# Optimization experiments

Hardware: AMD Instinct MI355X
Metric: run time of the kernel (lower is better)

## Reference

```python
import jax, jax.numpy as jnp
import numpy as np

B, T, S, E, H, F = 4, 1024, 1024, 512, 8, 2048
D = E // H  # head_dim = 64
SCALE = D ** -0.5
EPS = 1e-5


def setup_inputs() -> dict:
    key = jax.random.key(0)
    ks = jax.random.split(key, 16)
    w = lambda k, shape: jax.random.normal(k, shape, jnp.float32) * 0.02
    inp = {
        'tgt': jax.random.normal(ks[0], (B, T, E), jnp.float32),
        'memory': jax.random.normal(ks[1], (B, S, E), jnp.float32),
    }
    for i, n in enumerate(['sWq', 'sWk', 'sWv', 'sWo', 'cWq', 'cWk', 'cWv', 'cWo']):
        inp[n] = w(ks[2 + i], (E, E))
    for n in ['sbq', 'sbk', 'sbv', 'sbo', 'cbq', 'cbk', 'cbv', 'cbo']:
        inp[n] = jnp.zeros((E,), jnp.float32)
    inp['fW1'] = w(ks[10], (E, F)); inp['fb1'] = jnp.zeros((F,), jnp.float32)
    inp['fW2'] = w(ks[11], (F, E)); inp['fb2'] = jnp.zeros((E,), jnp.float32)
    for n in ['g1', 'g2', 'g3']:
        inp[n] = jnp.ones((E,), jnp.float32)
    for n in ['be1', 'be2', 'be3']:
        inp[n] = jnp.zeros((E,), jnp.float32)
    return inp


def _ln(x, g, b):
    mu = jnp.mean(x, axis=-1, keepdims=True)
    var = jnp.mean(jnp.square(x - mu), axis=-1, keepdims=True)
    return (x - mu) * jax.lax.rsqrt(var + EPS) * g + b


def _mha(xq, xkv, Wq, bq, Wk, bk, Wv, bv, Wo, bo):
    # dense-equivalent of full N^2 edge-list attention (softmax over source nodes per target)
    Bq, Tq, _ = xq.shape
    Skv = xkv.shape[1]
    q = (xq @ Wq + bq).reshape(Bq, Tq, H, D)
    k = (xkv @ Wk + bk).reshape(Bq, Skv, H, D)
    v = (xkv @ Wv + bv).reshape(Bq, Skv, H, D)
    scores = jnp.einsum('bthd,bshd->bhts', q, k) * SCALE
    wts = jax.nn.softmax(scores, axis=-1)
    out = jnp.einsum('bhts,bshd->bthd', wts, v).reshape(Bq, Tq, E)
    return out @ Wo + bo


def reference(tgt, memory,
              sWq, sbq, sWk, sbk, sWv, sbv, sWo, sbo,
              cWq, cbq, cWk, cbk, cWv, cbv, cWo, cbo,
              fW1, fb1, fW2, fb2,
              g1, be1, g2, be2, g3, be3):
    # post-norm decoder layer: self-attn -> cross-attn -> FFN (dropout=0 eval)
    x = _ln(tgt + _mha(tgt, tgt, sWq, sbq, sWk, sbk, sWv, sbv, sWo, sbo), g1, be1)
    x = _ln(x + _mha(x, memory, cWq, cbq, cWk, cbk, cWv, cbv, cWo, cbo), g2, be2)
    ff = jax.nn.relu(x @ fW1 + fb1) @ fW2 + fb2
    x = _ln(x + ff, g3, be3)
    return x
```

## Files before the change

### kernel.cpp

```cpp
#include <hip/hip_runtime.h>

typedef unsigned short ushort_t;
typedef short short8 __attribute__((ext_vector_type(8)));
typedef float float4v __attribute__((ext_vector_type(4)));

__device__ __forceinline__ float bf2f(ushort_t u) {
    union { unsigned int i; float f; } x; x.i = ((unsigned int)u) << 16; return x.f;
}
__device__ __forceinline__ ushort_t f2bf(float f) {
    unsigned int u = __float_as_uint(f);
    unsigned int r = (u + 0x7FFFu + ((u >> 16) & 1u)) >> 16;
    return (ushort_t)r;
}
__device__ __forceinline__ void store_out(float* p, float v) { *p = v; }
__device__ __forceinline__ void store_out(ushort_t* p, float v) { *p = f2bf(v); }

__device__ __forceinline__ void gll16(const ushort_t* g, ushort_t* l) {
    __builtin_amdgcn_global_load_lds(
        (const __attribute__((address_space(1))) void*)g,
        (__attribute__((address_space(3))) void*)l, 16, 0, 0);
}

__global__ void detect_dtype(const ushort_t* __restrict__ tgt, int* __restrict__ flag) {
    __shared__ int red[256];
    const int tid = threadIdx.x;
    int p = 0;
    for (int i = tid; i < 512; i += 256) {
        ushort_t u = tgt[i];
        int e = (u >> 7) & 0xFF;
        if (u == 0 || (e >= 100 && e <= 140)) ++p;
    }
    red[tid] = p; __syncthreads();
    for (int off = 128; off > 0; off >>= 1) {
        if (tid < off) red[tid] += red[tid + off];
        __syncthreads();
    }
    if (tid == 0) flag[0] = (red[0] >= 480) ? 1 : 0;
}

__global__ __launch_bounds__(256) void wtrans_all(
    const void* sWq, const void* sWk, const void* sWv, const void* sWo,
    const void* cWq, const void* cWk, const void* cWv, const void* cWo,
    const void* fW1, const void* fW2,
    ushort_t* __restrict__ wb, const int* __restrict__ dflag)
{
    const void* src; ushort_t* dst; int Kd, Nd;
    switch (blockIdx.z) {
        case 0: src = sWq; dst = wb + 0;       Kd = 512;  Nd = 512;  break;
        case 1: src = sWk; dst = wb + 262144;  Kd = 512;  Nd = 512;  break;
        case 2: src = sWv; dst = wb + 524288;  Kd = 512;  Nd = 512;  break;
        case 3: src = sWo; dst = wb + 786432;  Kd = 512;  Nd = 512;  break;
        case 4: src = cWq; dst = wb + 1048576; Kd = 512;  Nd = 512;  break;
        case 5: src = cWk; dst = wb + 1310720; Kd = 512;  Nd = 512;  break;
        case 6: src = cWv; dst = wb + 1572864; Kd = 512;  Nd = 512;  break;
        case 7: src = cWo; dst = wb + 1835008; Kd = 512;  Nd = 512;  break;
        case 8: src = fW1; dst = wb + 2097152; Kd = 512;  Nd = 2048; break;
        default:src = fW2; dst = wb + 3145728; Kd = 2048; Nd = 512;  break;
    }
    const int k0 = blockIdx.x * 64, n0 = blockIdx.y * 64;
    if (k0 >= Kd || n0 >= Nd) return;
    const bool f32 = (dflag[0] == 0);
    __shared__ ushort_t T[64][65];
    const int tid = threadIdx.x;
#pragma unroll
    for (int i = 0; i < 16; ++i) {
        int j = i * 256 + tid;
        int r = j >> 6, c = j & 63;
        float v = f32 ? ((const float*)src)[(size_t)(k0 + r) * Nd + n0 + c]
                      : bf2f(((const ushort_t*)src)[(size_t)(k0 + r) * Nd + n0 + c]);
        T[r][c] = f2bf(v);
    }
    __syncthreads();
#pragma unroll
    for (int i = 0; i < 16; ++i) {
        int j = i * 256 + tid;
        int n = j >> 6, k = j & 63;
        dst[(size_t)(n0 + n) * Kd + k0 + k] = T[k][n];
    }
}

__global__ __launch_bounds__(256) void conv_act(
    const void* __restrict__ t, const void* __restrict__ m,
    ushort_t* __restrict__ td, ushort_t* __restrict__ md,
    const int* __restrict__ dflag)
{
    const bool f32 = (dflag[0] == 0);
    const void* src = blockIdx.y ? m : t;
    ushort_t* dst = blockIdx.y ? md : td;
    const int i = (blockIdx.x * 256 + threadIdx.x) * 4;
    if (f32) {
        float4 v = *(const float4*)((const float*)src + i);
        ushort_t o[4] = { f2bf(v.x), f2bf(v.y), f2bf(v.z), f2bf(v.w) };
        *(uint2*)(dst + i) = *(const uint2*)o;
    } else {
        *(uint2*)(dst + i) = *(const uint2*)((const ushort_t*)src + i);
    }
}

__global__ __launch_bounds__(256) void prep_bias(
    const void* sbq, const void* sbk, const void* sbv, const void* sbo,
    const void* cbq, const void* cbk, const void* cbv, const void* cbo,
    const void* fb1, const void* fb2,
    float* __restrict__ dst, const int* __restrict__ dflag)
{
    const bool f32 = (dflag[0] == 0);
    const int i = blockIdx.x * 256 + threadIdx.x;
    if (i >= 6656) return;
    const void* src; int off;
    if      (i < 512)  { src = sbq; off = i; }
    else if (i < 1024) { src = sbk; off = i - 512; }
    else if (i < 1536) { src = sbv; off = i - 1024; }
    else if (i < 2048) { src = sbo; off = i - 1536; }
    else if (i < 2560) { src = cbq; off = i - 2048; }
    else if (i < 3072) { src = cbk; off = i - 2560; }
    else if (i < 3584) { src = cbv; off = i - 3072; }
    else if (i < 4096) { src = cbo; off = i - 3584; }
    else if (i < 6144) { src = fb1; off = i - 4096; }
    else               { src = fb2; off = i - 6144; }
    dst[i] = f32 ? ((const float*)src)[off] : bf2f(((const ushort_t*)src)[off]);
}

template<typename OutT, bool RELU, int BN>
__global__ __launch_bounds__(256) void gemm_tn(
    const ushort_t* __restrict__ A1, const ushort_t* __restrict__ A2,
    int ySplit, int lda,
    const ushort_t* __restrict__ Wt, int ldw,
    const float* __restrict__ bias,
    OutT* __restrict__ C, int ldc, int K)
{
    constexpr int MI = (BN == 128) ? 4 : 2;
    __shared__ ushort_t As[128][64];
    __shared__ ushort_t Bs[BN][64];
    const int tid = threadIdx.x;
    const int wave = tid >> 6, lane = tid & 63;
    const int quad = lane >> 4, l16 = lane & 15;
    const int m0 = blockIdx.x * 128, n0 = blockIdx.y * BN;
    const int wm = (BN == 128) ? (wave >> 1) * 64 : wave * 32;
    const int wn = (BN == 128) ? (wave & 1) * 64 : 0;
    const ushort_t* A = (((int)blockIdx.y) < ySplit) ? A1 : A2;

    float4v acc[MI][4];
#pragma unroll
    for (int mi = 0; mi < MI; ++mi)
#pragma unroll
        for (int ni = 0; ni < 4; ++ni) {
            acc[mi][ni][0] = 0.f; acc[mi][ni][1] = 0.f;
            acc[mi][ni][2] = 0.f; acc[mi][ni][3] = 0.f;
        }

    const int lr = lane >> 3;
    const int lcsw = ((lane & 7) ^ lr) * 8;
    const ushort_t* aptr = A  + (size_t)(m0 + wave * 8 + lr) * lda + lcsw;
    const ushort_t* bptr = Wt + (size_t)(n0 + wave * 8 + lr) * ldw + lcsw;
    ushort_t* asl = &As[wave * 8][0];
    ushort_t* bsl = &Bs[wave * 8][0];
    const int xsw = (l16 & 7);

    for (int k0 = 0; k0 < K; k0 += 64) {
#pragma unroll
        for (int j = 0; j < 4; ++j)
            gll16(aptr + (size_t)(j * 32) * lda, asl + j * 32 * 64);
#pragma unroll
        for (int j = 0; j < BN / 32; ++j)
            gll16(bptr + (size_t)(j * 32) * ldw, bsl + j * 32 * 64);
        aptr += 64; bptr += 64;
        __syncthreads();

#pragma unroll
        for (int ks = 0; ks < 2; ++ks) {
            const int ca = ((quad + ks * 4) ^ xsw) * 8;
            short8 af[MI], bfr[4];
#pragma unroll
            for (int mi = 0; mi < MI; ++mi)
                af[mi] = *(const short8*)(&As[wm + mi * 16 + l16][ca]);
#pragma unroll
            for (int ni = 0; ni < 4; ++ni)
                bfr[ni] = *(const short8*)(&Bs[wn + ni * 16 + l16][ca]);
#pragma unroll
            for (int mi = 0; mi < MI; ++mi)
#pragma unroll
                for (int ni = 0; ni < 4; ++ni)
                    acc[mi][ni] = __builtin_amdgcn_mfma_f32_16x16x32_bf16(
                        af[mi], bfr[ni], acc[mi][ni], 0, 0, 0);
        }
        __syncthreads();
    }

#pragma unroll
    for (int ni = 0; ni < 4; ++ni) {
        const int col = n0 + wn + ni * 16 + l16;
        const float bv = bias[col];
#pragma unroll
        for (int mi = 0; mi < MI; ++mi)
#pragma unroll
            for (int r = 0; r < 4; ++r) {
                const int row = m0 + wm + mi * 16 + quad * 4 + r;
                float v = acc[mi][ni][r] + bv;
                if (RELU) v = fmaxf(v, 0.f);
                store_out(&C[(size_t)row * ldc + col], v);
            }
    }
}

__global__ __launch_bounds__(256) void attn_mfma(ushort_t* __restrict__ QKV)
{
    const int S = 1536;
    __shared__ ushort_t Qs[64][72];
    __shared__ ushort_t Ks[64][72];
    __shared__ ushort_t Vt[64][72];
    __shared__ ushort_t Ps[4][16][72];

    const int tid  = threadIdx.x;
    const int wave = tid >> 6, lane = tid & 63;
    const int quad = lane >> 4, l16 = lane & 15;
    const int qt = blockIdx.x, bh = blockIdx.y;
    const int b = bh >> 3, h = bh & 7;
    const size_t rowQ = (size_t)b * 1024 + qt * 64;
    const size_t kv0  = (size_t)b * 1024;

    {
        const int r = tid >> 2, c = (tid & 3) * 16;
        const ushort_t* src = QKV + (rowQ + r) * S + h * 64 + c;
        *(uint4*)(&Qs[r][c])     = *(const uint4*)(src);
        *(uint4*)(&Qs[r][c + 8]) = *(const uint4*)(src + 8);
    }
    __syncthreads();
    short8 qf[2];
    qf[0] = *(const short8*)(&Qs[wave * 16 + l16][quad * 8]);
    qf[1] = *(const short8*)(&Qs[wave * 16 + l16][32 + quad * 8]);

    const float CEXP = 0.125f * 1.44269504f;
    const float MREF = 16.0f * CEXP;
    float lsum[4];
    float4v oacc[4];
#pragma unroll
    for (int r = 0; r < 4; ++r) lsum[r] = 0.f;
#pragma unroll
    for (int n = 0; n < 4; ++n) { oacc[n][0]=0.f; oacc[n][1]=0.f; oacc[n][2]=0.f; oacc[n][3]=0.f; }

    for (int s0 = 0; s0 < 1024; s0 += 64) {
        __syncthreads();
        {
            const int r = tid >> 2, c = (tid & 3) * 16;
            const ushort_t* ksrc = QKV + (kv0 + s0 + r) * S + 512 + h * 64 + c;
            *(uint4*)(&Ks[r][c])     = *(const uint4*)(ksrc);
            *(uint4*)(&Ks[r][c + 8]) = *(const uint4*)(ksrc + 8);
        }
        {
            const int sp = tid >> 3, dc = (tid & 7) * 8;
            const int r0 = sp * 2;
            const ushort_t* v0 = QKV + (kv0 + s0 + r0) * S + 1024 + h * 64 + dc;
            uint4 a = *(const uint4*)v0;
            uint4 bq = *(const uint4*)(v0 + S);
            const ushort_t* ae = (const ushort_t*)&a;
            const ushort_t* be = (const ushort_t*)&bq;
            const int rg = r0 >> 3, rof = r0 & 7;
#pragma unroll
            for (int j = 0; j < 8; ++j) {
                const int d = dc + j;
                const int cc = (rg ^ (d >> 4)) & 7;
                *(unsigned int*)(&Vt[d][cc * 8 + rof]) =
                    (unsigned int)ae[j] | ((unsigned int)be[j] << 16);
            }
        }
        __syncthreads();

        float4v sc[4];
#pragma unroll
        for (int sb = 0; sb < 4; ++sb) {
            float4v z; z[0]=0.f; z[1]=0.f; z[2]=0.f; z[3]=0.f;
            short8 kf0 = *(const short8*)(&Ks[sb * 16 + l16][quad * 8]);
            short8 kf1 = *(const short8*)(&Ks[sb * 16 + l16][32 + quad * 8]);
            z = __builtin_amdgcn_mfma_f32_16x16x32_bf16(qf[0], kf0, z, 0, 0, 0);
            z = __builtin_amdgcn_mfma_f32_16x16x32_bf16(qf[1], kf1, z, 0, 0, 0);
            sc[sb] = z;
        }

#pragma unroll
        for (int sb = 0; sb < 4; ++sb)
#pragma unroll
            for (int r = 0; r < 4; ++r) {
                float p = exp2f(fmaf(sc[sb][r], CEXP, -MREF));
                lsum[r] += p;
                Ps[wave][quad * 4 + r][sb * 16 + l16] = f2bf(p);
            }

        short8 pf[2];
        pf[0] = *(const short8*)(&Ps[wave][l16][quad * 8]);
        pf[1] = *(const short8*)(&Ps[wave][l16][32 + quad * 8]);
#pragma unroll
        for (int n = 0; n < 4; ++n) {
#pragma unroll
            for (int kc = 0; kc < 2; ++kc) {
                const int cc = ((kc * 4 + quad) ^ n) & 7;
                short8 vf = *(const short8*)(&Vt[n * 16 + l16][cc * 8]);
                oacc[n] = __builtin_amdgcn_mfma_f32_16x16x32_bf16(pf[kc], vf, oacc[n], 0, 0, 0);
            }
        }
    }

#pragma unroll
    for (int msk = 1; msk < 16; msk <<= 1)
#pragma unroll
        for (int r = 0; r < 4; ++r) lsum[r] += __shfl_xor(lsum[r], msk);
    float inv[4];
#pragma unroll
    for (int r = 0; r < 4; ++r) inv[r] = 1.f / lsum[r];
#pragma unroll
    for (int n = 0; n < 4; ++n)
#pragma unroll
        for (int r = 0; r < 4; ++r) {
            const size_t row = rowQ + wave * 16 + quad * 4 + r;
            QKV[row * S + h * 64 + n * 16 + l16] = f2bf(oacc[n][r] * inv[r]);
        }
}

template<bool RES_EXT, bool DELTA_F32, bool OUT_FLAG>
__global__ __launch_bounds__(256) void ln_kernel(
    const void* __restrict__ res, const void* __restrict__ delta,
    const void* __restrict__ g, const void* __restrict__ be,
    void* __restrict__ out, const int* __restrict__ dflag)
{
    const int E = 512;
    const bool extf32 = (dflag[0] == 0);
    const int row = blockIdx.x, tid = threadIdx.x;
    const int wave = tid >> 6, lane = tid & 63;
    const size_t base = (size_t)row * E;
    const int i0 = tid, i1 = tid + 256;

    float r0, r1;
    if (RES_EXT && extf32) {
        r0 = ((const float*)res)[base + i0];
        r1 = ((const float*)res)[base + i1];
    } else {
        r0 = bf2f(((const ushort_t*)res)[base + i0]);
        r1 = bf2f(((const ushort_t*)res)[base + i1]);
    }
    float d0v, d1v;
    if (DELTA_F32) {
        d0v = ((const float*)delta)[base + i0];
        d1v = ((const float*)delta)[base + i1];
    } else {
        d0v = bf2f(((const ushort_t*)delta)[base + i0]);
        d1v = bf2f(((const ushort_t*)delta)[base + i1]);
    }
    float x0 = r0 + d0v, x1 = r1 + d1v;

    __shared__ float red8[8];
    float s = x0 + x1;
#pragma unroll
    for (int m = 1; m < 64; m <<= 1) s += __shfl_xor(s, m);
    if (lane == 0) red8[wave] = s;
    __syncthreads();
    float mean = (red8[0] + red8[1] + red8[2] + red8[3]) * (1.0f / 512.0f);
    float dd0 = x0 - mean, dd1 = x1 - mean;
    float v = dd0 * dd0 + dd1 * dd1;
#pragma unroll
    for (int m = 1; m < 64; m <<= 1) v += __shfl_xor(v, m);
    if (lane == 0) red8[4 + wave] = v;
    __syncthreads();
    float rstd = rsqrtf((red8[4] + red8[5] + red8[6] + red8[7]) * (1.0f / 512.0f) + 1e-5f);

    float g0, g1v, b0, b1;
    if (extf32) {
        g0 = ((const float*)g)[i0];  g1v = ((const float*)g)[i1];
        b0 = ((const float*)be)[i0]; b1  = ((const float*)be)[i1];
    } else {
        g0 = bf2f(((const ushort_t*)g)[i0]);  g1v = bf2f(((const ushort_t*)g)[i1]);
        b0 = bf2f(((const ushort_t*)be)[i0]); b1  = bf2f(((const ushort_t*)be)[i1]);
    }
    float y0 = dd0 * rstd * g0 + b0;
    float y1 = dd1 * rstd * g1v + b1;
    if (OUT_FLAG && extf32) {
        ((float*)out)[base + i0] = y0; ((float*)out)[base + i1] = y1;
    } else {
        ((ushort_t*)out)[base + i0] = f2bf(y0);
        ((ushort_t*)out)[base + i1] = f2bf(y1);
    }
}


extern "C" void kernel_launch(void* const* d_in, const int* in_sizes, int n_in,
                              void* d_out, int out_size, void* d_ws, size_t ws_size,
                              hipStream_t stream) {
    const void* tgt = d_in[0];
    const void* mem = d_in[1];
    const void* sWq = d_in[2];  const void* sWk = d_in[3];
    const void* sWv = d_in[4];  const void* sWo = d_in[5];
    const void* cWq = d_in[6];  const void* cWk = d_in[7];
    const void* cWv = d_in[8];  const void* cWo = d_in[9];
    const void* sbq = d_in[10]; const void* sbk = d_in[11];
    const void* sbv = d_in[12]; const void* sbo = d_in[13];
    const void* cbq = d_in[14]; const void* cbk = d_in[15];
    const void* cbv = d_in[16]; const void* cbo = d_in[17];
    const void* fW1 = d_in[18]; const void* fb1 = d_in[19];
    const void* fW2 = d_in[20]; const void* fb2 = d_in[21];
    const void* g1  = d_in[22]; const void* g2  = d_in[23];
    const void* g3  = d_in[24];
    const void* be1 = d_in[25]; const void* be2 = d_in[26];
    const void* be3 = d_in[27];

    char* ws = (char*)d_ws;
    const size_t MB = 1048576;
    ushort_t* qkv = (ushort_t*)(ws + 0 * MB);
    ushort_t* hb  = (ushort_t*)(ws + 0 * MB);
    ushort_t* po  = (ushort_t*)(ws + 12 * MB);
    ushort_t* xb  = (ushort_t*)(ws + 16 * MB);
    ushort_t* tb  = (ushort_t*)(ws + 20 * MB);
    ushort_t* mb  = (ushort_t*)(ws + 24 * MB);
    float*    of  = (float*)   (ws + 20 * MB);
    ushort_t* wb  = (ushort_t*)(ws + 28 * MB);
    float*    pb  = (float*)   (ws + 36 * MB);
    int*   dflag  = (int*)     (ws + 36 * MB + 262144);

    const ushort_t* sWqkv_t = wb + 0;
    const ushort_t* sWo_t   = wb + 786432;
    const ushort_t* cWqkv_t = wb + 1048576;
    const ushort_t* cWo_t   = wb + 1835008;
    const ushort_t* fW1_t   = wb + 2097152;
    const ushort_t* fW2_t   = wb + 3145728;

    dim3 blk(256);

    detect_dtype<<<dim3(1), blk, 0, stream>>>((const ushort_t*)tgt, dflag);
    wtrans_all<<<dim3(32, 32, 10), blk, 0, stream>>>(sWq, sWk, sWv, sWo, cWq, cWk, cWv, cWo, fW1, fW2, wb, dflag);
    conv_act<<<dim3(2048, 2), blk, 0, stream>>>(tgt, mem, tb, mb, dflag);
    prep_bias<<<dim3(26), blk, 0, stream>>>(sbq, sbk, sbv, sbo, cbq, cbk, cbv, cbo, fb1, fb2, pb, dflag);

    dim3 gattn(16, 32);

    gemm_tn<ushort_t, false, 128><<<dim3(32, 12), blk, 0, stream>>>(tb, tb, 0, 512, sWqkv_t, 512, pb + 0, qkv, 1536, 512);
    attn_mfma<<<gattn, blk, 0, stream>>>(qkv);
    gemm_tn<ushort_t, false, 64><<<dim3(32, 8), blk, 0, stream>>>(qkv, qkv, 0, 1536, sWo_t, 512, pb + 1536, po, 512, 512);
    ln_kernel<true, false, false><<<dim3(4096), blk, 0, stream>>>(tgt, po, g1, be1, xb, dflag);

    gemm_tn<ushort_t, false, 128><<<dim3(32, 12), blk, 0, stream>>>(xb, mb, 4, 512, cWqkv_t, 512, pb + 2048, qkv, 1536, 512);
    attn_mfma<<<gattn, blk, 0, stream>>>(qkv);
    gemm_tn<ushort_t, false, 64><<<dim3(32, 8), blk, 0, stream>>>(qkv, qkv, 0, 1536, cWo_t, 512, pb + 3584, po, 512, 512);
    ln_kernel<false, false, false><<<dim3(4096), blk, 0, stream>>>(xb, po, g2, be2, xb, dflag);

    gemm_tn<ushort_t, true, 128><<<dim3(32, 16), blk, 0, stream>>>(xb, xb, 0, 512, fW1_t, 512, pb + 4096, hb, 2048, 512);
    gemm_tn<float, false, 64><<<dim3(32, 8), blk, 0, stream>>>(hb, hb, 0, 2048, fW2_t, 2048, pb + 6144, of, 512, 2048);
    ln_kernel<false, true, true><<<dim3(4096), blk, 0, stream>>>(xb, of, g3, be3, d_out, dflag);
}
```

Measured before the change: 308.6 us.

## Double-buffer GEMM K-loop with BK=32 and merge prep kernels into one launch

The GEMM main loop moves from a single 64-wide K tile with two barriers per step to a two-stage ping-pong LDS buffer of 32-wide K tiles. The next tile's global-to-LDS load is issued before the current tile's MFMAs, so each step needs one barrier and loads overlap compute. The weight transpose, activation conversion and bias prep kernels are merged into one launch, with activation conversion widened to 8 elements per thread. The tradeoff is a shorter K step, giving more loop iterations and barriers per FLOP, plus a new swizzle pattern.

Result: no change. 311.0 us (+0.8%).

```diff
diff --git a/kernel.cpp b/kernel.cpp
--- a/kernel.cpp
+++ b/kernel.cpp
@@ -38,86 +38,89 @@
     if (tid == 0) flag[0] = (red[0] >= 480) ? 1 : 0;
 }
 
-__global__ __launch_bounds__(256) void wtrans_all(
+__global__ __launch_bounds__(256) void prep_all(
     const void* sWq, const void* sWk, const void* sWv, const void* sWo,
     const void* cWq, const void* cWk, const void* cWv, const void* cWo,
     const void* fW1, const void* fW2,
-    ushort_t* __restrict__ wb, const int* __restrict__ dflag)
-{
-    const void* src; ushort_t* dst; int Kd, Nd;
-    switch (blockIdx.z) {
-        case 0: src = sWq; dst = wb + 0;       Kd = 512;  Nd = 512;  break;
-        case 1: src = sWk; dst = wb + 262144;  Kd = 512;  Nd = 512;  break;
-        case 2: src = sWv; dst = wb + 524288;  Kd = 512;  Nd = 512;  break;
-        case 3: src = sWo; dst = wb + 786432;  Kd = 512;  Nd = 512;  break;
-        case 4: src = cWq; dst = wb + 1048576; Kd = 512;  Nd = 512;  break;
-        case 5: src = cWk; dst = wb + 1310720; Kd = 512;  Nd = 512;  break;
-        case 6: src = cWv; dst = wb + 1572864; Kd = 512;  Nd = 512;  break;
-        case 7: src = cWo; dst = wb + 1835008; Kd = 512;  Nd = 512;  break;
-        case 8: src = fW1; dst = wb + 2097152; Kd = 512;  Nd = 2048; break;
-        default:src = fW2; dst = wb + 3145728; Kd = 2048; Nd = 512;  break;
-    }
-    const int k0 = blockIdx.x * 64, n0 = blockIdx.y * 64;
-    if (k0 >= Kd || n0 >= Nd) return;
-    const bool f32 = (dflag[0] == 0);
-    __shared__ ushort_t T[64][65];
-    const int tid = threadIdx.x;
-#pragma unroll
-    for (int i = 0; i < 16; ++i) {
-        int j = i * 256 + tid;
-        int r = j >> 6, c = j & 63;
-        float v = f32 ? ((const float*)src)[(size_t)(k0 + r) * Nd + n0 + c]
-                      : bf2f(((const ushort_t*)src)[(size_t)(k0 + r) * Nd + n0 + c]);
-        T[r][c] = f2bf(v);
-    }
-    __syncthreads();
-#pragma unroll
-    for (int i = 0; i < 16; ++i) {
-        int j = i * 256 + tid;
-        int n = j >> 6, k = j & 63;
-        dst[(size_t)(n0 + n) * Kd + k0 + k] = T[k][n];
-    }
-}
-
-__global__ __launch_bounds__(256) void conv_act(
-    const void* __restrict__ t, const void* __restrict__ m,
-    ushort_t* __restrict__ td, ushort_t* __restrict__ md,
-    const int* __restrict__ dflag)
-{
-    const bool f32 = (dflag[0] == 0);
-    const void* src = blockIdx.y ? m : t;
-    ushort_t* dst = blockIdx.y ? md : td;
-    const int i = (blockIdx.x * 256 + threadIdx.x) * 4;
-    if (f32) {
-        float4 v = *(const float4*)((const float*)src + i);
-        ushort_t o[4] = { f2bf(v.x), f2bf(v.y), f2bf(v.z), f2bf(v.w) };
-        *(uint2*)(dst + i) = *(const uint2*)o;
-    } else {
-        *(uint2*)(dst + i) = *(const uint2*)((const ushort_t*)src + i);
-    }
-}
-
-__global__ __launch_bounds__(256) void prep_bias(
+    const void* tgt, const void* mem,
     const void* sbq, const void* sbk, const void* sbv, const void* sbo,
     const void* cbq, const void* cbk, const void* cbv, const void* cbo,
     const void* fb1, const void* fb2,
-    float* __restrict__ dst, const int* __restrict__ dflag)
+    ushort_t* __restrict__ wb, ushort_t* __restrict__ tb, ushort_t* __restrict__ mb,
+    float* __restrict__ pb, const int* __restrict__ dflag)
 {
     const bool f32 = (dflag[0] == 0);
-    const int i = blockIdx.x * 256 + threadIdx.x;
-    if (i >= 6656) return;
-    const void* src; int off;
-    if      (i < 512)  { src = sbq; off = i; }
-    else if (i < 1024) { src = sbk; off = i - 512; }
-    else if (i < 1536) { src = sbv; off = i - 1024; }
-    else if (i < 2048) { src = sbo; off = i - 1536; }
-    else if (i < 2560) { src = cbq; off = i - 2048; }
-    else if (i < 3072) { src = cbk; off = i - 2560; }
-    else if (i < 3584) { src = cbv; off = i - 3072; }
-    else if (i < 4096) { src = cbo; off = i - 3584; }
-    else if (i < 6144) { src = fb1; off = i - 4096; }
-    else               { src = fb2; off = i - 6144; }
-    dst[i] = f32 ? ((const float*)src)[off] : bf2f(((const ushort_t*)src)[off]);
+    const int tid = threadIdx.x;
+    const int z = blockIdx.z;
+
+    if (z < 10) {
+        const void* src; ushort_t* dst; int Kd, Nd;
+        switch (z) {
+            case 0: src = sWq; dst = wb + 0;       Kd = 512;  Nd = 512;  break;
+            case 1: src = sWk; dst = wb + 262144;  Kd = 512;  Nd = 512;  break;
+            case 2: src = sWv; dst = wb + 524288;  Kd = 512;  Nd = 512;  break;
+            case 3: src = sWo; dst = wb + 786432;  Kd = 512;  Nd = 512;  break;
+            case 4: src = cWq; dst = wb + 1048576; Kd = 512;  Nd = 512;  break;
+            case 5: src = cWk; dst = wb + 1310720; Kd = 512;  Nd = 512;  break;
+            case 6: src = cWv; dst = wb + 1572864; Kd = 512;  Nd = 512;  break;
+            case 7: src = cWo; dst = wb + 1835008; Kd = 512;  Nd = 512;  break;
+            case 8: src = fW1; dst = wb + 2097152; Kd = 512;  Nd = 2048; break;
+            default:src = fW2; dst = wb + 3145728; Kd = 2048; Nd = 512;  break;
+        }
+        const int k0 = blockIdx.x * 64, n0 = blockIdx.y * 64;
+        if (k0 >= Kd || n0 >= Nd) return;
+        __shared__ ushort_t T[64][65];
+#pragma unroll
+        for (int i = 0; i < 16; ++i) {
+            int j = i * 256 + tid;
+            int r = j >> 6, c = j & 63;
+            float v = f32 ? ((const float*)src)[(size_t)(k0 + r) * Nd + n0 + c]
+                          : bf2f(((const ushort_t*)src)[(size_t)(k0 + r) * Nd + n0 + c]);
+            T[r][c] = f2bf(v);
+        }
+        __syncthreads();
+#pragma unroll
+        for (int i = 0; i < 16; ++i) {
+            int j = i * 256 + tid;
+            int n = j >> 6, k = j & 63;
+            dst[(size_t)(n0 + n) * Kd + k0 + k] = T[k][n];
+        }
+        return;
+    }
+
+    const int bid = blockIdx.x * 32 + blockIdx.y;
+    if (z < 12) {
+        const void* src = (z == 10) ? tgt : mem;
+        ushort_t* dst = (z == 10) ? tb : mb;
+        const int i = (bid * 256 + tid) * 8;
+        if (f32) {
+            float4 v0 = *(const float4*)((const float*)src + i);
+            float4 v1 = *(const float4*)((const float*)src + i + 4);
+            ushort_t o[8] = { f2bf(v0.x), f2bf(v0.y), f2bf(v0.z), f2bf(v0.w),
+                              f2bf(v1.x), f2bf(v1.y), f2bf(v1.z), f2bf(v1.w) };
+            *(uint4*)(dst + i) = *(const uint4*)o;
+        } else {
+            *(uint4*)(dst + i) = *(const uint4*)((const ushort_t*)src + i);
+        }
+        return;
+    }
+
+    {
+        const int i = bid * 256 + tid;
+        if (bid >= 26 || i >= 6656) return;
+        const void* src; int off;
+        if      (i < 512)  { src = sbq; off = i; }
+        else if (i < 1024) { src = sbk; off = i - 512; }
+        else if (i < 1536) { src = sbv; off = i - 1024; }
+        else if (i < 2048) { src = sbo; off = i - 1536; }
+        else if (i < 2560) { src = cbq; off = i - 2048; }
+        else if (i < 3072) { src = cbk; off = i - 2560; }
+        else if (i < 3584) { src = cbv; off = i - 3072; }
+        else if (i < 4096) { src = cbo; off = i - 3584; }
+        else if (i < 6144) { src = fb1; off = i - 4096; }
+        else               { src = fb2; off = i - 6144; }
+        pb[i] = f32 ? ((const float*)src)[off] : bf2f(((const ushort_t*)src)[off]);
+    }
 }
 
 template<typename OutT, bool RELU, int BN>
@@ -129,8 +132,8 @@
     OutT* __restrict__ C, int ldc, int K)
 {
     constexpr int MI = (BN == 128) ? 4 : 2;
-    __shared__ ushort_t As[128][64];
-    __shared__ ushort_t Bs[BN][64];
+    __shared__ ushort_t As[2][128][32];
+    __shared__ ushort_t Bs[2][BN][32];
     const int tid = threadIdx.x;
     const int wave = tid >> 6, lane = tid & 63;
     const int quad = lane >> 4, l16 = lane & 15;
@@ -148,42 +151,44 @@
             acc[mi][ni][2] = 0.f; acc[mi][ni][3] = 0.f;
         }
 
-    const int lr = lane >> 3;
-    const int lcsw = ((lane & 7) ^ lr) * 8;
-    const ushort_t* aptr = A  + (size_t)(m0 + wave * 8 + lr) * lda + lcsw;
-    const ushort_t* bptr = Wt + (size_t)(n0 + wave * 8 + lr) * ldw + lcsw;
-    ushort_t* asl = &As[wave * 8][0];
-    ushort_t* bsl = &Bs[wave * 8][0];
-    const int xsw = (l16 & 7);
-
-    for (int k0 = 0; k0 < K; k0 += 64) {
-#pragma unroll
-        for (int j = 0; j < 4; ++j)
-            gll16(aptr + (size_t)(j * 32) * lda, asl + j * 32 * 64);
-#pragma unroll
-        for (int j = 0; j < BN / 32; ++j)
-            gll16(bptr + (size_t)(j * 32) * ldw, bsl + j * 32 * 64);
-        aptr += 64; bptr += 64;
+    const int srow = lane >> 2;
+    const int scc  = lane & 3;
+    const int sg   = (scc - (lane >> 3)) & 3;
+    const ushort_t* aptr0 = A  + (size_t)(m0 + wave * 16 + srow) * lda + sg * 8;
+    const ushort_t* aptr1 = A  + (size_t)(m0 + 64 + wave * 16 + srow) * lda + sg * 8;
+    const ushort_t* bptr0 = Wt + (size_t)(n0 + wave * 16 + srow) * ldw + sg * 8;
+    const ushort_t* bptr1 = Wt + (size_t)(n0 + 64 + wave * 16 + srow) * ldw + sg * 8;
+
+    gll16(aptr0, &As[0][wave * 16][0]);
+    gll16(aptr1, &As[0][64 + wave * 16][0]);
+    gll16(bptr0, &Bs[0][wave * 16][0]);
+    if (BN == 128) gll16(bptr1, &Bs[0][64 + wave * 16][0]);
+
+    const int ca = ((quad + (l16 >> 1)) & 3) * 8;
+    int cur = 0;
+    for (int k0 = 0; k0 < K; k0 += 32) {
         __syncthreads();
-
-#pragma unroll
-        for (int ks = 0; ks < 2; ++ks) {
-            const int ca = ((quad + ks * 4) ^ xsw) * 8;
-            short8 af[MI], bfr[4];
-#pragma unroll
-            for (int mi = 0; mi < MI; ++mi)
-                af[mi] = *(const short8*)(&As[wm + mi * 16 + l16][ca]);
+        if (k0 + 32 < K) {
+            const int nb = cur ^ 1, ko = k0 + 32;
+            gll16(aptr0 + ko, &As[nb][wave * 16][0]);
+            gll16(aptr1 + ko, &As[nb][64 + wave * 16][0]);
+            gll16(bptr0 + ko, &Bs[nb][wave * 16][0]);
+            if (BN == 128) gll16(bptr1 + ko, &Bs[nb][64 + wave * 16][0]);
+        }
+        short8 af[MI], bfr[4];
+#pragma unroll
+        for (int mi = 0; mi < MI; ++mi)
+            af[mi] = *(const short8*)(&As[cur][wm + mi * 16 + l16][ca]);
+#pragma unroll
+        for (int ni = 0; ni < 4; ++ni)
+            bfr[ni] = *(const short8*)(&Bs[cur][wn + ni * 16 + l16][ca]);
+#pragma unroll
+        for (int mi = 0; mi < MI; ++mi)
 #pragma unroll
             for (int ni = 0; ni < 4; ++ni)
-                bfr[ni] = *(const short8*)(&Bs[wn + ni * 16 + l16][ca]);
-#pragma unroll
-            for (int mi = 0; mi < MI; ++mi)
-#pragma unroll
-                for (int ni = 0; ni < 4; ++ni)
-                    acc[mi][ni] = __builtin_amdgcn_mfma_f32_16x16x32_bf16(
-                        af[mi], bfr[ni], acc[mi][ni], 0, 0, 0);
-        }
-        __syncthreads();
+                acc[mi][ni] = __builtin_amdgcn_mfma_f32_16x16x32_bf16(
+                    af[mi], bfr[ni], acc[mi][ni], 0, 0, 0);
+        cur ^= 1;
     }
 
 #pragma unroll
@@ -423,9 +428,10 @@
     dim3 blk(256);
 
     detect_dtype<<<dim3(1), blk, 0, stream>>>((const ushort_t*)tgt, dflag);
-    wtrans_all<<<dim3(32, 32, 10), blk, 0, stream>>>(sWq, sWk, sWv, sWo, cWq, cWk, cWv, cWo, fW1, fW2, wb, dflag);
-    conv_act<<<dim3(2048, 2), blk, 0, stream>>>(tgt, mem, tb, mb, dflag);
-    prep_bias<<<dim3(26), blk, 0, stream>>>(sbq, sbk, sbv, sbo, cbq, cbk, cbv, cbo, fb1, fb2, pb, dflag);
+    prep_all<<<dim3(32, 32, 13), blk, 0, stream>>>(
+        sWq, sWk, sWv, sWo, cWq, cWk, cWv, cWo, fW1, fW2,
+        tgt, mem, sbq, sbk, sbv, sbo, cbq, cbk, cbv, cbo, fb1, fb2,
+        wb, tb, mb, pb, dflag);
 
     dim3 gattn(16, 32);
 
```
